# Optimization experiments

Measured on AMD Instinct MI355X. Metric: run time of the kernel, lower is better.

Reference implementation:

```python
import jax, jax.numpy as jnp
import numpy as np

LN_EPS = 1e-5


def _layernorm(x, g, b):
    mu = jnp.mean(x, axis=-1, keepdims=True)
    var = jnp.mean(jnp.square(x - mu), axis=-1, keepdims=True)
    return (x - mu) * jax.lax.rsqrt(var + LN_EPS) * g + b


def setup_inputs() -> dict:
    key = jax.random.key(0)
    ks = jax.random.split(key, 4)
    B, N, C = 32, 512, 1024
    return {
        "r": jax.random.normal(ks[0], (B, N, C), dtype=jnp.float32),
        "ln_gamma": jnp.ones((C,), dtype=jnp.float32),
        "ln_beta": jnp.zeros((C,), dtype=jnp.float32),
        "qkv_w": jax.random.normal(ks[1], (C, 3 * C), dtype=jnp.float32) * (C ** -0.5),
        "qkv_b": jnp.zeros((3 * C,), dtype=jnp.float32),
        "proj_w": jax.random.normal(ks[2], (C, C), dtype=jnp.float32) * (C ** -0.5),
        "proj_b": jnp.zeros((C,), dtype=jnp.float32),
        "sig_w": jax.random.normal(ks[3], (C, C), dtype=jnp.float32) * (C ** -0.5),
        "sig_b": jnp.zeros((C,), dtype=jnp.float32),
        "num_heads": 16,
        "latent_num": 64,
    }


def reference(r, ln_gamma, ln_beta, qkv_w, qkv_b, proj_w, proj_b, sig_w, sig_b,
              num_heads, latent_num):
    B, N, C = r.shape
    H = num_heads
    D = C // H
    scale = D ** -0.5

    x = _layernorm(r, ln_gamma, ln_beta)
    qkv = (x @ qkv_w + qkv_b).reshape(B, N, 3, H, D)
    q, k, v = jnp.moveaxis(qkv, 2, 0)              # each (B, N, H, D)
    q = jnp.transpose(q, (0, 2, 1, 3))             # (B, H, N, D)
    k = jnp.transpose(k, (0, 2, 1, 3))
    v = jnp.transpose(v, (0, 2, 1, 3))

    attn = jax.nn.softmax(jnp.einsum('bhnd,bhmd->bhnm', q, k) * scale, axis=-1)
    out = jnp.einsum('bhnm,bhmd->bhnd', attn, v)   # (B, H, N, D)
    out = jnp.transpose(out, (0, 2, 1, 3)).reshape(B, N, C)
    out = out @ proj_w + proj_b

    out = out + out                                 # r + DropPath(r), eval -> Identity
    agg = jnp.mean(out, axis=1)                     # (B, C)
    mu = jnp.mean(agg, axis=0, keepdims=True)       # (1, C)
    sigma = 0.1 + 0.9 * jax.nn.sigmoid(mu @ sig_w + sig_b)  # (1, C)

    eps = jax.random.normal(jax.random.key(42), (latent_num, 1, C), dtype=r.dtype)
    latent = jnp.squeeze(mu + sigma * eps, axis=1)  # (latent_num, C)
    return latent
```

## Files before the change

### kernel.cpp

```cpp
#include <hip/hip_runtime.h>

#define B_ 32
#define N_ 512
#define C_ 1024
#define H_ 16
#define D_ 64
#define TC_ 3072
#define NQK_ 2048
#define M_ (B_*N_)

typedef unsigned int u32;
typedef unsigned short u16;
typedef __attribute__((ext_vector_type(8))) unsigned short ushort8;
typedef __attribute__((ext_vector_type(8))) short bf16x8;
typedef __attribute__((ext_vector_type(4))) float f32x4;

__device__ __forceinline__ float bfl(u32 u){ return __builtin_bit_cast(float, u << 16); }
__device__ __forceinline__ u16 f2bf(float f){
  u32 u = __builtin_bit_cast(u32, f);
  u32 r = (u + 0x7FFFu + ((u >> 16) & 1u)) >> 16;
  return (u16)r;
}

__global__ __launch_bounds__(256) void k_pre(const float* __restrict__ r,
                                             const float* __restrict__ g,
                                             const float* __restrict__ be,
                                             const float* __restrict__ W,
                                             u16* __restrict__ X,
                                             u16* __restrict__ WT) {
  __shared__ float tile[32][33];
  int bid = blockIdx.x, t = threadIdx.x;
  if (bid < M_) {
    float* red = &tile[0][0];
    int row = bid;
    float4 v = ((const float4*)(r + (size_t)row * C_))[t];
    float s = (v.x + v.y) + (v.z + v.w);
    #pragma unroll
    for (int o = 32; o; o >>= 1) s += __shfl_xor(s, o);
    if ((t & 63) == 0) red[t >> 6] = s;
    __syncthreads();
    float mean = (red[0] + red[1] + red[2] + red[3]) * (1.f / 1024.f);
    float d0 = v.x - mean, d1 = v.y - mean, d2 = v.z - mean, d3 = v.w - mean;
    float q = d0*d0 + d1*d1 + d2*d2 + d3*d3;
    #pragma unroll
    for (int o = 32; o; o >>= 1) q += __shfl_xor(q, o);
    if ((t & 63) == 0) red[4 + (t >> 6)] = q;
    __syncthreads();
    float var = (red[4] + red[5] + red[6] + red[7]) * (1.f / 1024.f);
    float rs = rsqrtf(var + 1e-5f);
    float4 gv = ((const float4*)g)[t];
    float4 bv = ((const float4*)be)[t];
    ushort4 o4;
    o4.x = f2bf(d0 * rs * gv.x + bv.x);
    o4.y = f2bf(d1 * rs * gv.y + bv.y);
    o4.z = f2bf(d2 * rs * gv.z + bv.z);
    o4.w = f2bf(d3 * rs * gv.w + bv.w);
    ((ushort4*)X)[(size_t)row * 256 + t] = o4;
  } else {
    int wb = bid - M_;
    int k0 = (wb & 31) * 32, n0 = (wb >> 5) * 32;
    int rr = t >> 3, c4 = (t & 7) * 4;
    float4 v = *(const float4*)(W + (size_t)(k0 + rr) * TC_ + n0 + c4);
    tile[rr][c4] = v.x; tile[rr][c4 + 1] = v.y; tile[rr][c4 + 2] = v.z; tile[rr][c4 + 3] = v.w;
    __syncthreads();
    int n = t >> 3, k4 = (t & 7) * 4;
    ushort4 o;
    o.x = f2bf(tile[k4][n]);     o.y = f2bf(tile[k4 + 1][n]);
    o.z = f2bf(tile[k4 + 2][n]); o.w = f2bf(tile[k4 + 3][n]);
    *(ushort4*)(WT + (size_t)(n0 + n) * C_ + k0 + k4) = o;
  }
}

__global__ __launch_bounds__(256) void k_qk(const u16* __restrict__ X,
                                            const u16* __restrict__ WT,
                                            const float* __restrict__ bias,
                                            u16* __restrict__ QK) {
  __shared__ u16 As[128 * 32];
  __shared__ u16 Bs[128 * 32];
  int t = threadIdx.x, lane = t & 63, w = t >> 6;
  int wr = w >> 1, wc = w & 1;
  int bid = blockIdx.x;
  int swz = (bid & 7) * 256 + (bid >> 3);
  int rowA0 = (swz >> 4) * 128, colB0 = (swz & 15) * 128;
  int colbase = lane & 15, kslot = lane >> 4;

  f32x4 acc[4][4] = {};

  for (int k0 = 0; k0 < C_; k0 += 32) {
    __syncthreads();
    const u16* Xrow = X + (size_t)rowA0 * C_ + k0;
    const u16* Wrow = WT + (size_t)colB0 * C_ + k0;
    #pragma unroll
    for (int p = 0; p < 2; p++) {
      int o = p * 4096 + w * 1024 + lane * 16;
      int row = o >> 6, slot = (o >> 4) & 3;
      int kb16 = slot ^ ((row >> 1) & 3);
      const u16* gp = Xrow + (size_t)row * C_ + (kb16 << 3);
      __builtin_amdgcn_global_load_lds((const __attribute__((address_space(1))) void*)gp,
                                       (__attribute__((address_space(3))) void*)((char*)As + o),
                                       16, 0, 0);
    }
    #pragma unroll
    for (int p = 0; p < 2; p++) {
      int o = p * 4096 + w * 1024 + lane * 16;
      int row = o >> 6, slot = (o >> 4) & 3;
      int kb16 = slot ^ ((row >> 1) & 3);
      const u16* gp = Wrow + (size_t)row * C_ + (kb16 << 3);
      __builtin_amdgcn_global_load_lds((const __attribute__((address_space(1))) void*)gp,
                                       (__attribute__((address_space(3))) void*)((char*)Bs + o),
                                       16, 0, 0);
    }
    __syncthreads();
    bf16x8 a[4], b[4];
    #pragma unroll
    for (int i = 0; i < 4; i++) {
      int row = wr * 64 + i * 16 + colbase;
      a[i] = *(const bf16x8*)((const char*)As + row * 64 + ((kslot ^ ((row >> 1) & 3)) << 4));
    }
    #pragma unroll
    for (int j = 0; j < 4; j++) {
      int col = wc * 64 + j * 16 + colbase;
      b[j] = *(const bf16x8*)((const char*)Bs + col * 64 + ((kslot ^ ((col >> 1) & 3)) << 4));
    }
    #pragma unroll
    for (int i = 0; i < 4; i++)
      #pragma unroll
      for (int j = 0; j < 4; j++)
        acc[i][j] = __builtin_amdgcn_mfma_f32_16x16x32_bf16(a[i], b[j], acc[i][j], 0, 0, 0);
  }

  float bv[4];
  #pragma unroll
  for (int j = 0; j < 4; j++) bv[j] = bias[colB0 + wc * 64 + j * 16 + colbase];
  #pragma unroll
  for (int i = 0; i < 4; i++) {
    #pragma unroll
    for (int j = 0; j < 4; j++) {
      int col = colB0 + wc * 64 + j * 16 + colbase;
      int tsel = col >> 10, rem = col & 1023;
      int h = rem >> 6, dd = rem & 63;
      #pragma unroll
      for (int q = 0; q < 4; q++) {
        int m = rowA0 + wr * 64 + i * 16 + (lane >> 4) * 4 + q;
        int b2 = m >> 9, n = m & 511;
        QK[(((size_t)(tsel * B_ + b2) * H_ + h) * N_ + n) * D_ + dd] = f2bf(acc[i][j][q] + bv[j]);
      }
    }
  }
}

__global__ __launch_bounds__(512) void k_attn(const u16* __restrict__ QK,
                                              float* __restrict__ CWg) {
  __shared__ u16 Ks[N_ * D_];
  __shared__ float rsl[N_];
  int bh = blockIdx.x;
  const u16* qb = QK + (size_t)bh * (N_ * D_);
  const u16* kb = QK + (size_t)(B_ * H_ + bh) * (N_ * D_);
  int t = threadIdx.x, lane = t & 63, w = t >> 6;
  int colbase = lane & 15, kslot = lane >> 4;

  #pragma unroll
  for (int i2 = 0; i2 < 8; i2++) {
    int vec = t + i2 * 512;
    int c = vec >> 3, d8 = vec & 7;
    uint4 pk = *(const uint4*)(kb + ((size_t)c << 6) + (d8 << 3));
    *(uint4*)((char*)Ks + c * 128 + ((d8 ^ (c & 7)) << 4)) = pk;
  }
  __syncthreads();

  #pragma unroll 1
  for (int si = 0; si < 4; si++) {
    int n0 = (w * 4 + si) * 16;
    bf16x8 aq0 = *(const bf16x8*)(qb + (size_t)(n0 + colbase) * 64 + kslot * 8);
    bf16x8 aq1 = *(const bf16x8*)(qb + (size_t)(n0 + colbase) * 64 + 32 + kslot * 8);
    float sj[4] = {0.f, 0.f, 0.f, 0.f};
    #pragma unroll 4
    for (int tl = 0; tl < 32; tl++) {
      int m = tl * 16 + colbase;
      const char* kr = (const char*)Ks + m * 128;
      bf16x8 bk0 = *(const bf16x8*)(kr + ((kslot ^ (m & 7)) << 4));
      bf16x8 bk1 = *(const bf16x8*)(kr + (((kslot + 4) ^ (m & 7)) << 4));
      f32x4 z = {0.f, 0.f, 0.f, 0.f};
      z = __builtin_amdgcn_mfma_f32_16x16x32_bf16(aq0, bk0, z, 0, 0, 0);
      z = __builtin_amdgcn_mfma_f32_16x16x32_bf16(aq1, bk1, z, 0, 0, 0);
      #pragma unroll
      for (int q = 0; q < 4; q++) sj[q] += __expf(z[q] * 0.125f);
    }
    #pragma unroll
    for (int q = 0; q < 4; q++) {
      sj[q] += __shfl_xor(sj[q], 1);
      sj[q] += __shfl_xor(sj[q], 2);
      sj[q] += __shfl_xor(sj[q], 4);
      sj[q] += __shfl_xor(sj[q], 8);
    }
    if (colbase == 0) {
      #pragma unroll
      for (int q = 0; q < 4; q++) rsl[n0 + kslot * 4 + q] = 1.f / sj[q];
    }
  }
  __syncthreads();

  bf16x8 kf[4][2];
  #pragma unroll
  for (int ct = 0; ct < 4; ct++) {
    int m = (w * 4 + ct) * 16 + colbase;
    const char* kr = (const char*)Ks + m * 128;
    kf[ct][0] = *(const bf16x8*)(kr + ((kslot ^ (m & 7)) << 4));
    kf[ct][1] = *(const bf16x8*)(kr + (((kslot + 4) ^ (m & 7)) << 4));
  }
  f32x4 acc[4] = {};
  #pragma unroll 2
  for (int si = 0; si < 32; si++) {
    int n0 = si * 16;
    bf16x8 aq0 = *(const bf16x8*)(qb + (size_t)(n0 + colbase) * 64 + kslot * 8);
    bf16x8 aq1 = *(const bf16x8*)(qb + (size_t)(n0 + colbase) * 64 + 32 + kslot * 8);
    float rr = rsl[n0 + colbase];
    #pragma unroll
    for (int ct = 0; ct < 4; ct++) {
      f32x4 z = {0.f, 0.f, 0.f, 0.f};
      z = __builtin_amdgcn_mfma_f32_16x16x32_bf16(kf[ct][0], aq0, z, 0, 0, 0);
      z = __builtin_amdgcn_mfma_f32_16x16x32_bf16(kf[ct][1], aq1, z, 0, 0, 0);
      #pragma unroll
      for (int q = 0; q < 4; q++) acc[ct][q] += __expf(z[q] * 0.125f) * rr;
    }
  }
  #pragma unroll
  for (int ct = 0; ct < 4; ct++) {
    #pragma unroll
    for (int q = 0; q < 4; q++) {
      float v = acc[ct][q];
      v += __shfl_xor(v, 1);
      v += __shfl_xor(v, 2);
      v += __shfl_xor(v, 4);
      v += __shfl_xor(v, 8);
      if (colbase == 0)
        CWg[(size_t)bh * 512 + (w * 4 + ct) * 16 + kslot * 4 + q] = v * (1.f / 512.f);
    }
  }
}

__global__ __launch_bounds__(256) void k_ybar(const float* __restrict__ CW,
                                              const u16* __restrict__ X,
                                              float* __restrict__ Y2) {
  __shared__ float cwl[256][17];
  int bid = blockIdx.x;
  int kb = bid & 7, b = (bid >> 3) & 31, mh = bid >> 8;
  int t = threadIdx.x;
  int h = t >> 4, ks = t & 15;
  int m0 = mh * 256;
  #pragma unroll
  for (int i = 0; i < 16; i++)
    cwl[t][i] = CW[(size_t)(b * 16 + i) * 512 + m0 + t];
  __syncthreads();
  int kc = kb * 128 + ks * 8;
  const u16* Xb = X + ((size_t)b * 512 + m0) * 1024 + kc;
  float acc[8] = {};
  #pragma unroll 4
  for (int m = 0; m < 256; m++) {
    float wgt = cwl[m][h];
    ushort8 xv = *(const ushort8*)(Xb + (size_t)m * 1024);
    #pragma unroll
    for (int e = 0; e < 8; e++) acc[e] = fmaf(wgt, bfl((u32)xv[e]), acc[e]);
  }
  float* yp = Y2 + ((size_t)(mh * 32 + b) * 16 + h) * 1024 + kc;
  *(float4*)yp = *(float4*)&acc[0];
  *(float4*)(yp + 4) = *(float4*)&acc[4];
}

__global__ __launch_bounds__(256) void k_head0(const float* __restrict__ y,
                                               const float* __restrict__ qkvw,
                                               float* __restrict__ zp) {
  __shared__ float yb[256];
  __shared__ float part[4][64];
  int blk = blockIdx.x;
  int h = blk >> 2, q = blk & 3;
  int t = threadIdx.x;
  int k0 = q * 256;
  {
    float s = 0.f;
    int k = k0 + t;
    #pragma unroll 8
    for (int p = 0; p < 64; p++) s += y[((size_t)(p * 16 + h) << 10) + k];
    yb[t] = s * (1.f / 32.f);
  }
  __syncthreads();
  int col = t & 63, g = t >> 6;
  float acc = 0.f;
  #pragma unroll 8
  for (int kk = 0; kk < 64; kk++) {
    int k = g * 64 + kk;
    acc = fmaf(yb[k], qkvw[(size_t)(k0 + k) * TC_ + 2048 + h * 64 + col], acc);
  }
  part[g][col] = acc;
  __syncthreads();
  if (t < 64)
    zp[(size_t)q * 1024 + h * 64 + t] = part[0][t] + part[1][t] + part[2][t] + part[3][t];
}

__global__ __launch_bounds__(256) void k_head1(const float* __restrict__ zp,
                                               const float* __restrict__ qkvb,
                                               const float* __restrict__ pw,
                                               const float* __restrict__ pb,
                                               float* __restrict__ mu) {
  __shared__ float zs[1024];
  __shared__ float part[8][32];
  int t = threadIdx.x;
  for (int j = t; j < 1024; j += 256)
    zs[j] = zp[j] + zp[1024 + j] + zp[2048 + j] + zp[3072 + j] + qkvb[2048 + j];
  __syncthreads();
  int col = blockIdx.x * 32 + (t & 31), q = t >> 5;
  float acc = 0.f;
  #pragma unroll 4
  for (int k = q * 128; k < q * 128 + 128; k++)
    acc = fmaf(zs[k], pw[(size_t)k * 1024 + col], acc);
  part[q][t & 31] = acc;
  __syncthreads();
  if (t < 32) {
    float s = pb[blockIdx.x * 32 + t];
    #pragma unroll
    for (int p = 0; p < 8; p++) s += part[p][t];
    mu[blockIdx.x * 32 + t] = 2.f * s;
  }
}

__device__ __forceinline__ uint2 threefry_0_42(u32 x0, u32 x1) {
  const u32 ks0 = 0u, ks1 = 42u, ks2 = 0x1BD11BF0u;
  x0 += ks0; x1 += ks1;
  #define RND(r) { x0 += x1; x1 = (x1 << r) | (x1 >> (32 - r)); x1 ^= x0; }
  RND(13) RND(15) RND(26) RND(6)   x0 += ks1; x1 += ks2 + 1u;
  RND(17) RND(29) RND(16) RND(24)  x0 += ks2; x1 += ks0 + 2u;
  RND(13) RND(15) RND(26) RND(6)   x0 += ks0; x1 += ks1 + 3u;
  RND(17) RND(29) RND(16) RND(24)  x0 += ks1; x1 += ks2 + 4u;
  RND(13) RND(15) RND(26) RND(6)   x0 += ks2; x1 += ks0 + 5u;
  #undef RND
  return make_uint2(x0, x1);
}

__device__ __forceinline__ float bits_to_normal(u32 bits) {
  u32 fb = (bits >> 9) | 0x3F800000u;
  float fl = __builtin_bit_cast(float, fb) - 1.0f;
  float u = __fmul_rn(fl, 2.0f);
  u = __fadd_rn(u, -0.99999994f);
  u = fmaxf(-0.99999994f, u);
  float x = u;
  float wv = -log1pf(-x * x);
  float p;
  if (wv < 5.0f) {
    wv -= 2.5f;
    p = 2.81022636e-08f;
    p = fmaf(p, wv, 3.43273939e-07f);
    p = fmaf(p, wv, -3.5233877e-06f);
    p = fmaf(p, wv, -4.39150654e-06f);
    p = fmaf(p, wv, 0.00021858087f);
    p = fmaf(p, wv, -0.00125372503f);
    p = fmaf(p, wv, -0.00417768164f);
    p = fmaf(p, wv, 0.246640727f);
    p = fmaf(p, wv, 1.50140941f);
  } else {
    wv = sqrtf(wv) - 3.0f;
    p = -0.000200214257f;
    p = fmaf(p, wv, 0.000100950558f);
    p = fmaf(p, wv, 0.00134934322f);
    p = fmaf(p, wv, -0.00367342844f);
    p = fmaf(p, wv, 0.00573950773f);
    p = fmaf(p, wv, -0.0076224613f);
    p = fmaf(p, wv, 0.00943887047f);
    p = fmaf(p, wv, 1.00167406f);
    p = fmaf(p, wv, 2.83297682f);
  }
  return 1.41421356f * (p * x);
}

__global__ __launch_bounds__(256) void k_head2(const float* __restrict__ mu,
                                               const float* __restrict__ sw,
                                               const float* __restrict__ sb,
                                               float* __restrict__ out) {
  __shared__ float ms[1024];
  __shared__ float part[8][32];
  __shared__ float sigs[32];
  int t = threadIdx.x;
  for (int j = t; j < 1024; j += 256) ms[j] = mu[j];
  __syncthreads();
  int col = blockIdx.x * 32 + (t & 31), q = t >> 5;
  float acc = 0.f;
  #pragma unroll 4
  for (int k = q * 128; k < q * 128 + 128; k++)
    acc = fmaf(ms[k], sw[(size_t)k * 1024 + col], acc);
  part[q][t & 31] = acc;
  __syncthreads();
  if (t < 32) {
    float s = sb[blockIdx.x * 32 + t];
    #pragma unroll
    for (int p = 0; p < 8; p++) s += part[p][t];
    sigs[t] = 0.1f + 0.9f / (1.f + expf(-s));
  }
  __syncthreads();
  int c0 = blockIdx.x * 32;
  #pragma unroll
  for (int e = t; e < 64 * 32; e += 256) {
    int row = e >> 5, cc = e & 31;
    u32 f = (u32)row * 1024 + c0 + cc;
    uint2 rb = threefry_0_42(0u, f);
    float eps = bits_to_normal(rb.x ^ rb.y);
    out[f] = ms[c0 + cc] + sigs[cc] * eps;
  }
}

extern "C" void kernel_launch(void* const* d_in, const int* in_sizes, int n_in,
                              void* d_out, int out_size, void* d_ws, size_t ws_size,
                              hipStream_t stream) {
  const float* r    = (const float*)d_in[0];
  const float* lng  = (const float*)d_in[1];
  const float* lnb  = (const float*)d_in[2];
  const float* qkvw = (const float*)d_in[3];
  const float* qkvb = (const float*)d_in[4];
  const float* pw   = (const float*)d_in[5];
  const float* pb   = (const float*)d_in[6];
  const float* sw   = (const float*)d_in[7];
  const float* sb   = (const float*)d_in[8];
  float* out = (float*)d_out;

  u16* X   = (u16*)d_ws;
  u16* QK  = X + (size_t)M_ * C_;
  u16* WT  = QK + (size_t)2 * M_ * C_;
  float* CW = (float*)(WT + (size_t)NQK_ * C_);
  float* Y2 = CW + (size_t)B_ * H_ * N_;
  float* ZP = Y2 + (size_t)64 * H_ * C_;
  float* MU = ZP + 4 * C_;

  k_pre<<<M_ + NQK_, 256, 0, stream>>>(r, lng, lnb, qkvw, X, WT);
  k_qk<<<M_ / 128 * (NQK_ / 128), 256, 0, stream>>>(X, WT, qkvb, QK);
  k_attn<<<B_ * H_, 512, 0, stream>>>(QK, CW);
  k_ybar<<<512, 256, 0, stream>>>(CW, X, Y2);
  k_head0<<<64, 256, 0, stream>>>(Y2, qkvw, ZP);
  k_head1<<<32, 256, 0, stream>>>(ZP, qkvb, pw, pb, MU);
  k_head2<<<32, 256, 0, stream>>>(MU, sw, sb, out);
}
```

Baseline: 231.8 us.

## Triple-buffer QK GEMM LDS tiles with async prefetch two stages ahead

Turns the QK projection GEMM's single-buffered LDS staging into a three-stage ring. Each step issues direct-to-LDS global loads for the tile two steps ahead, then waits with an explicit vmcnt count so only the current tile must be resident. This lets global memory latency overlap with the MFMA work instead of stalling at every K step. In exchange it triples the LDS footprint for this kernel, which may reduce occupancy, and it relies on hand-placed waitcnt and barrier ordering being correct.

```diff
diff --git a/kernel.cpp b/kernel.cpp
--- a/kernel.cpp
+++ b/kernel.cpp
@@ -20,6 +20,12 @@
   u32 u = __builtin_bit_cast(u32, f);
   u32 r = (u + 0x7FFFu + ((u >> 16) & 1u)) >> 16;
   return (u16)r;
+}
+
+#define FENCE() asm volatile("" ::: "memory")
+#define RAWBAR() { FENCE(); __builtin_amdgcn_s_barrier(); FENCE(); }
+template<int N> __device__ __forceinline__ void vmwait() {
+  asm volatile("s_waitcnt vmcnt(%0)" :: "n"(N) : "memory");
 }
 
 __global__ __launch_bounds__(256) void k_pre(const float* __restrict__ r,
@@ -75,8 +81,8 @@
                                             const u16* __restrict__ WT,
                                             const float* __restrict__ bias,
                                             u16* __restrict__ QK) {
-  __shared__ u16 As[128 * 32];
-  __shared__ u16 Bs[128 * 32];
+  __shared__ u16 As[3][128 * 32];
+  __shared__ u16 Bs[3][128 * 32];
   int t = threadIdx.x, lane = t & 63, w = t >> 6;
   int wr = w >> 1, wc = w & 1;
   int bid = blockIdx.x;
@@ -86,41 +92,50 @@
 
   f32x4 acc[4][4] = {};
 
-  for (int k0 = 0; k0 < C_; k0 += 32) {
-    __syncthreads();
-    const u16* Xrow = X + (size_t)rowA0 * C_ + k0;
-    const u16* Wrow = WT + (size_t)colB0 * C_ + k0;
-    #pragma unroll
-    for (int p = 0; p < 2; p++) {
-      int o = p * 4096 + w * 1024 + lane * 16;
-      int row = o >> 6, slot = (o >> 4) & 3;
-      int kb16 = slot ^ ((row >> 1) & 3);
-      const u16* gp = Xrow + (size_t)row * C_ + (kb16 << 3);
-      __builtin_amdgcn_global_load_lds((const __attribute__((address_space(1))) void*)gp,
-                                       (__attribute__((address_space(3))) void*)((char*)As + o),
-                                       16, 0, 0);
-    }
-    #pragma unroll
-    for (int p = 0; p < 2; p++) {
-      int o = p * 4096 + w * 1024 + lane * 16;
-      int row = o >> 6, slot = (o >> 4) & 3;
-      int kb16 = slot ^ ((row >> 1) & 3);
-      const u16* gp = Wrow + (size_t)row * C_ + (kb16 << 3);
-      __builtin_amdgcn_global_load_lds((const __attribute__((address_space(1))) void*)gp,
-                                       (__attribute__((address_space(3))) void*)((char*)Bs + o),
-                                       16, 0, 0);
-    }
-    __syncthreads();
+  int o0 = w * 1024 + lane * 16;
+  int o1 = 4096 + w * 1024 + lane * 16;
+  int r0 = o0 >> 6, s0 = (o0 >> 4) & 3, kb0 = s0 ^ ((r0 >> 1) & 3);
+  int r1 = o1 >> 6, s1 = (o1 >> 4) & 3, kb1 = s1 ^ ((r1 >> 1) & 3);
+
+#define PF(buf, kt_) {                                                                 \
+    const u16* Xr = X + (size_t)rowA0 * C_ + (kt_) * 32;                               \
+    const u16* Wr = WT + (size_t)colB0 * C_ + (kt_) * 32;                              \
+    __builtin_amdgcn_global_load_lds(                                                  \
+      (const __attribute__((address_space(1))) void*)(Xr + (size_t)r0 * C_ + (kb0 << 3)), \
+      (__attribute__((address_space(3))) void*)((char*)As[buf] + o0), 16, 0, 0);       \
+    __builtin_amdgcn_global_load_lds(                                                  \
+      (const __attribute__((address_space(1))) void*)(Xr + (size_t)r1 * C_ + (kb1 << 3)), \
+      (__attribute__((address_space(3))) void*)((char*)As[buf] + o1), 16, 0, 0);       \
+    __builtin_amdgcn_global_load_lds(                                                  \
+      (const __attribute__((address_space(1))) void*)(Wr + (size_t)r0 * C_ + (kb0 << 3)), \
+      (__attribute__((address_space(3))) void*)((char*)Bs[buf] + o0), 16, 0, 0);       \
+    __builtin_amdgcn_global_load_lds(                                                  \
+      (const __attribute__((address_space(1))) void*)(Wr + (size_t)r1 * C_ + (kb1 << 3)), \
+      (__attribute__((address_space(3))) void*)((char*)Bs[buf] + o1), 16, 0, 0);       \
+  }
+
+  PF(0, 0);
+  PF(1, 1);
+
+  #pragma unroll
+  for (int kt = 0; kt < 32; kt++) {
+    RAWBAR();
+    if (kt + 2 < 32) PF((kt + 2) % 3, kt + 2);
+    if (kt + 2 < 32)      vmwait<8>();
+    else if (kt + 1 < 32) vmwait<4>();
+    else                  vmwait<0>();
+    RAWBAR();
+    const int buf = kt % 3;
     bf16x8 a[4], b[4];
     #pragma unroll
     for (int i = 0; i < 4; i++) {
       int row = wr * 64 + i * 16 + colbase;
-      a[i] = *(const bf16x8*)((const char*)As + row * 64 + ((kslot ^ ((row >> 1) & 3)) << 4));
+      a[i] = *(const bf16x8*)((const char*)As[buf] + row * 64 + ((kslot ^ ((row >> 1) & 3)) << 4));
     }
     #pragma unroll
     for (int j = 0; j < 4; j++) {
       int col = wc * 64 + j * 16 + colbase;
-      b[j] = *(const bf16x8*)((const char*)Bs + col * 64 + ((kslot ^ ((col >> 1) & 3)) << 4));
+      b[j] = *(const bf16x8*)((const char*)Bs[buf] + col * 64 + ((kslot ^ ((col >> 1) & 3)) << 4));
     }
     #pragma unroll
     for (int i = 0; i < 4; i++)
@@ -128,6 +143,7 @@
       for (int j = 0; j < 4; j++)
         acc[i][j] = __builtin_amdgcn_mfma_f32_16x16x32_bf16(a[i], b[j], acc[i][j], 0, 0, 0);
   }
+#undef PF
 
   float bv[4];
   #pragma unroll
```

Measured after the change: 225.9 us. 2.5% less time.
